# Optimization experiments

Measured on AMD Instinct MI355X. Metric: run time of the kernel, lower is better.

Reference implementation:

```python
import jax, jax.numpy as jnp
import numpy as np
from jax import lax

TAU = 10.0
THR = 1.0
ALPHA = float(np.exp(-1.0 / TAU))  # leak factor exp(-dt/tau), dt=1


def conv2d(x, w, pad):
    # x: [N,C,H,W], w: [O,I,kh,kw]
    return lax.conv_general_dilated(
        x, w, window_strides=(1, 1), padding=[(pad, pad), (pad, pad)],
        dimension_numbers=('NCHW', 'OIHW', 'NCHW'))


def avgpool(x, k):
    n, c, h, w = x.shape
    return x.reshape(n, c, h // k, k, w // k, k).mean(axis=(3, 5))


def exp_leak(x):
    # x: [T, ...]; v[t] = alpha*v[t-1] + x[t]; outputs membrane each step
    def step(v, xt):
        v = ALPHA * v + xt
        return v, v
    _, y = lax.scan(step, jnp.zeros_like(x[0]), x)
    return y


def lif(x):
    # LIF with SingleSpike + MembraneSubtract reset (norm_input=False)
    def step(v, xt):
        v = ALPHA * v + xt
        s = (v >= THR).astype(v.dtype)
        return v - s * THR, s
    _, s = lax.scan(step, jnp.zeros_like(x[0]), x)
    return s


def forward(x, conv1_w, conv2_w, lin_w):
    B, T = x.shape[:2]
    h = avgpool(conv2d(x.reshape(B * T, 2, 32, 32), conv1_w, 2), 4)  # [BT,4,8,8]
    h = h.reshape(B, T, 4, 8, 8).swapaxes(0, 1)                       # [T,B,4,8,8]
    h = lif(exp_leak(h)).swapaxes(0, 1).reshape(B * T, 4, 8, 8)
    h = avgpool(conv2d(h, conv2_w, 1), 2)                             # [BT,8,4,4]
    h = h.reshape(B, T, 8, 4, 4).swapaxes(0, 1)                       # [T,B,8,4,4]
    h = lif(exp_leak(h)).swapaxes(0, 1).reshape(B, T, 8 * 4 * 4)      # [B,T,128]
    return jnp.einsum('btf,of->bto', h, lin_w)                        # [B,T,2]


def setup_inputs() -> dict:
    key = jax.random.key(0)
    k1, k2, k3, k4 = jax.random.split(key, 4)
    B, T = 128, 100
    x = jax.random.uniform(k1, (B, T, 2, 32, 32), dtype=jnp.float32)
    conv1_w = jax.random.normal(k2, (4, 2, 5, 5), dtype=jnp.float32) / np.sqrt(2 * 5 * 5)
    conv2_w = jax.random.normal(k3, (8, 4, 3, 3), dtype=jnp.float32) / np.sqrt(4 * 3 * 3)
    lin_w = jax.random.normal(k4, (2, 128), dtype=jnp.float32) / np.sqrt(128)
    return {'x': x, 'conv1_w': conv1_w, 'conv2_w': conv2_w, 'lin_w': lin_w}


def reference(x, conv1_w, conv2_w, lin_w):
    return forward(x, conv1_w, conv2_w, lin_w)
```

## Files before the change

### kernel.cpp

```cpp
#include <hip/hip_runtime.h>

#define ALPHA 0.90483741803595957f

__global__ void prep_weights(const float* __restrict__ w1, const float* __restrict__ w2,
                             float* __restrict__ w1e, float* __restrict__ w2e) {
    int idx = blockIdx.x * 256 + threadIdx.x;
    if (idx < 512) {
        int v = idx & 7, u = (idx >> 3) & 7, ch = (idx >> 6) & 1, oc = idx >> 7;
        float s = 0.f;
        for (int a = 0; a < 5; ++a) {
            int i = u - a; if (i < 0 || i > 3) continue;
            for (int b = 0; b < 5; ++b) {
                int j = v - b; if (j < 0 || j > 3) continue;
                s += w1[((oc * 2 + ch) * 5 + a) * 5 + b];
            }
        }
        w1e[idx] = s * (1.f / 16.f);
    } else if (idx < 1024) {
        int k = idx - 512;
        int v = k & 3, u = (k >> 2) & 3, ch = (k >> 4) & 3, oc = k >> 6;
        float s = 0.f;
        for (int a = 0; a < 3; ++a) {
            int i = u - a; if (i < 0 || i > 1) continue;
            for (int b = 0; b < 3; ++b) {
                int j = v - b; if (j < 0 || j > 1) continue;
                s += w2[((oc * 4 + ch) * 3 + a) * 3 + b];
            }
        }
        w2e[k] = s * 0.25f;
    }
}

__global__ __launch_bounds__(256) void conv1_pool(const float* __restrict__ x,
                                                  const float* __restrict__ w1e,
                                                  float* __restrict__ y1) {
    __shared__ __align__(16) float tile[4][2][36][36];
    int tid = threadIdx.x;

    float4* t4 = (float4*)&tile[0][0][0][0];
    #pragma unroll
    for (int k = 0; k < 11; ++k) {
        int i = tid + k * 256;
        if (i < 2592) t4[i] = make_float4(0.f, 0.f, 0.f, 0.f);
    }
    __syncthreads();

    int li = tid >> 6, pos = tid & 63;
    long gi = (long)blockIdx.x * 4 + li;
    const float* src = x + gi * 2048;
    #pragma unroll
    for (int k = 0; k < 8; ++k) {
        int e = k * 256 + pos * 4;
        float4 d = *(const float4*)(src + e);
        int ch = e >> 10, rem = e & 1023, r = rem >> 5, c = rem & 31;
        float* dst = &tile[li][ch][r + 2][c + 2];
        dst[0] = d.x; dst[1] = d.y; dst[2] = d.z; dst[3] = d.w;
    }
    __syncthreads();

    int p = pos >> 3, q = pos & 7;
    float acc0 = 0.f, acc1 = 0.f, acc2 = 0.f, acc3 = 0.f;
    #pragma unroll
    for (int ch = 0; ch < 2; ++ch) {
        #pragma unroll
        for (int r = 0; r < 8; ++r) {
            const float* row = &tile[li][ch][4 * p + r][4 * q];
            float4 a = *(const float4*)row;
            float4 b = *(const float4*)(row + 4);
            float in[8] = {a.x, a.y, a.z, a.w, b.x, b.y, b.z, b.w};
            #pragma unroll
            for (int c = 0; c < 8; ++c) {
                float xi = in[c];
                acc0 += w1e[((0 * 2 + ch) * 8 + r) * 8 + c] * xi;
                acc1 += w1e[((1 * 2 + ch) * 8 + r) * 8 + c] * xi;
                acc2 += w1e[((2 * 2 + ch) * 8 + r) * 8 + c] * xi;
                acc3 += w1e[((3 * 2 + ch) * 8 + r) * 8 + c] * xi;
            }
        }
    }
    float* dst = y1 + gi * 256 + pos;
    dst[0] = acc0; dst[64] = acc1; dst[128] = acc2; dst[192] = acc3;
}

__global__ void scan1(const float* __restrict__ y1, float* __restrict__ spk) {
    int idx = blockIdx.x * 256 + threadIdx.x;
    int b = idx >> 8, f = idx & 255;
    const float* p = y1 + (long)b * 100 * 256 + f;
    float* o = spk + (long)b * 100 * 256 + f;
    float v1 = 0.f, v2 = 0.f;
    float xt = p[0];
    #pragma unroll 5
    for (int t = 0; t < 100; ++t) {
        float xn = (t < 99) ? p[(t + 1) * 256] : 0.f;
        v1 = ALPHA * v1 + xt;
        v2 = ALPHA * v2 + v1;
        float s = (v2 >= 1.f) ? 1.f : 0.f;
        o[t * 256] = s;
        v2 -= s;
        xt = xn;
    }
}

__global__ __launch_bounds__(256) void conv2_pool(const float* __restrict__ spk,
                                                  const float* __restrict__ w2e,
                                                  float* __restrict__ y2) {
    __shared__ __align__(16) float tile[2][4][10][10];
    int tid = threadIdx.x;
    float4* t4 = (float4*)&tile[0][0][0][0];
    if (tid < 200) t4[tid] = make_float4(0.f, 0.f, 0.f, 0.f);
    __syncthreads();

    const float* src = spk + (long)blockIdx.x * 512;
    #pragma unroll
    for (int k = 0; k < 2; ++k) {
        int e = k * 256 + tid;
        float d = src[e];
        int li = e >> 8, f = e & 255, ch = f >> 6, rem = f & 63, r = rem >> 3, c = rem & 7;
        tile[li][ch][r + 1][c + 1] = d;
    }
    __syncthreads();

    int li = tid >> 7, tpos = tid & 127;
    int oc = tpos >> 4, p = (tpos >> 2) & 3, q = tpos & 3;
    float acc = 0.f;
    #pragma unroll
    for (int ch = 0; ch < 4; ++ch) {
        #pragma unroll
        for (int r = 0; r < 4; ++r) {
            const float* row = &tile[li][ch][2 * p + r][2 * q];
            #pragma unroll
            for (int c = 0; c < 4; ++c)
                acc += w2e[((oc * 4 + ch) * 4 + r) * 4 + c] * row[c];
        }
    }
    long gi = (long)blockIdx.x * 2 + li;
    y2[gi * 128 + tpos] = acc;
}

__global__ void scan2(const float* __restrict__ y2, float* __restrict__ s2) {
    int idx = blockIdx.x * 256 + threadIdx.x;
    int b = idx >> 7, f = idx & 127;
    const float* p = y2 + (long)b * 100 * 128 + f;
    float* o = s2 + (long)b * 100 * 128 + f;
    float v1 = 0.f, v2 = 0.f;
    float xt = p[0];
    #pragma unroll 5
    for (int t = 0; t < 100; ++t) {
        float xn = (t < 99) ? p[(t + 1) * 128] : 0.f;
        v1 = ALPHA * v1 + xt;
        v2 = ALPHA * v2 + v1;
        float s = (v2 >= 1.f) ? 1.f : 0.f;
        o[t * 128] = s;
        v2 -= s;
        xt = xn;
    }
}

__global__ __launch_bounds__(256) void linear_out(const float* __restrict__ s2,
                                                  const float* __restrict__ lw,
                                                  float* __restrict__ out) {
    int tid = threadIdx.x;
    long bt = (long)blockIdx.x * 4 + (tid >> 6);
    int lane = tid & 63;
    float2 v = *(const float2*)(s2 + bt * 128 + lane * 2);
    float w00 = lw[lane * 2], w01 = lw[lane * 2 + 1];
    float w10 = lw[128 + lane * 2], w11 = lw[128 + lane * 2 + 1];
    float a0 = v.x * w00 + v.y * w01;
    float a1 = v.x * w10 + v.y * w11;
    #pragma unroll
    for (int off = 32; off; off >>= 1) {
        a0 += __shfl_down(a0, off);
        a1 += __shfl_down(a1, off);
    }
    if (lane == 0) { out[bt * 2] = a0; out[bt * 2 + 1] = a1; }
}

extern "C" void kernel_launch(void* const* d_in, const int* in_sizes, int n_in,
                              void* d_out, int out_size, void* d_ws, size_t ws_size,
                              hipStream_t stream) {
    const float* x  = (const float*)d_in[0];
    const float* w1 = (const float*)d_in[1];
    const float* w2 = (const float*)d_in[2];
    const float* lw = (const float*)d_in[3];
    float* out = (float*)d_out;

    float* ws   = (float*)d_ws;
    float* w1e  = ws;
    float* w2e  = ws + 512;
    float* bufA = ws + 1024;
    float* bufB = bufA + 3276800;

    prep_weights<<<4, 256, 0, stream>>>(w1, w2, w1e, w2e);
    conv1_pool<<<3200, 256, 0, stream>>>(x, w1e, bufA);
    scan1<<<128, 256, 0, stream>>>(bufA, bufB);
    conv2_pool<<<6400, 256, 0, stream>>>(bufB, w2e, bufA);
    scan2<<<64, 256, 0, stream>>>(bufA, bufB);
    linear_out<<<3200, 256, 0, stream>>>(bufB, lw, out);
}
```

Before: 209.7 us.

## Fuse scan1, conv2+pool, scan2 and linear into one per-batch kernel

Replaces the four post-conv1 kernels with one kernel, one block per batch element, that steps through time. Each step runs the first LIF scan, writes spikes to shared memory, computes conv2+pool from weights held in registers, runs the second scan, and applies the linear layer one step later on a double-buffered spike array. This removes the global round-trips of the intermediate spike and conv2 tensors and three launches. In exchange it serialises 100 timesteps with two block barriers each and runs only 128 blocks, so per-step latency and low occupancy may dominate.

```diff
diff --git a/kernel.cpp b/kernel.cpp
--- a/kernel.cpp
+++ b/kernel.cpp
@@ -82,97 +82,91 @@
     dst[0] = acc0; dst[64] = acc1; dst[128] = acc2; dst[192] = acc3;
 }
 
-__global__ void scan1(const float* __restrict__ y1, float* __restrict__ spk) {
-    int idx = blockIdx.x * 256 + threadIdx.x;
-    int b = idx >> 8, f = idx & 255;
-    const float* p = y1 + (long)b * 100 * 256 + f;
-    float* o = spk + (long)b * 100 * 256 + f;
-    float v1 = 0.f, v2 = 0.f;
-    float xt = p[0];
-    #pragma unroll 5
-    for (int t = 0; t < 100; ++t) {
-        float xn = (t < 99) ? p[(t + 1) * 256] : 0.f;
-        v1 = ALPHA * v1 + xt;
-        v2 = ALPHA * v2 + v1;
-        float s = (v2 >= 1.f) ? 1.f : 0.f;
-        o[t * 256] = s;
-        v2 -= s;
-        xt = xn;
+__global__ __launch_bounds__(256) void fused_rest(const float* __restrict__ y1,
+                                                  const float* __restrict__ w2e,
+                                                  const float* __restrict__ lw,
+                                                  float* __restrict__ out) {
+    __shared__ __align__(16) float spk[4][10][10];
+    __shared__ __align__(16) float s2buf[2][128];
+    __shared__ __align__(16) float outbuf[100][2];
+    int tid = threadIdx.x;
+    int b = blockIdx.x;
+
+    for (int i = tid; i < 400; i += 256) ((float*)spk)[i] = 0.f;
+
+    float wreg[64];
+    int g = tid, oc = g >> 4, p = (g >> 2) & 3, q = g & 3;
+    if (tid < 128) {
+        const float4* wsrc = (const float4*)(w2e + oc * 64);
+        #pragma unroll
+        for (int k = 0; k < 16; ++k) {
+            float4 w = wsrc[k];
+            wreg[4 * k] = w.x; wreg[4 * k + 1] = w.y;
+            wreg[4 * k + 2] = w.z; wreg[4 * k + 3] = w.w;
+        }
     }
-}
+    int lane = tid & 63;
+    float lwa = 0.f, lwb = 0.f;
+    if (tid >= 128) {
+        int o = (tid >> 6) - 2;
+        float2 lv = *(const float2*)(lw + o * 128 + 2 * lane);
+        lwa = lv.x; lwb = lv.y;
+    }
 
-__global__ __launch_bounds__(256) void conv2_pool(const float* __restrict__ spk,
-                                                  const float* __restrict__ w2e,
-                                                  float* __restrict__ y2) {
-    __shared__ __align__(16) float tile[2][4][10][10];
-    int tid = threadIdx.x;
-    float4* t4 = (float4*)&tile[0][0][0][0];
-    if (tid < 200) t4[tid] = make_float4(0.f, 0.f, 0.f, 0.f);
+    const float* yp = y1 + (long)b * 25600 + tid;
+    float v1a = 0.f, v1b = 0.f, v2a = 0.f, v2b = 0.f;
+    int ch = tid >> 6, r = (tid >> 3) & 7, c = tid & 7;
+
+    float xt = yp[0];
     __syncthreads();
 
-    const float* src = spk + (long)blockIdx.x * 512;
-    #pragma unroll
-    for (int k = 0; k < 2; ++k) {
-        int e = k * 256 + tid;
-        float d = src[e];
-        int li = e >> 8, f = e & 255, ch = f >> 6, rem = f & 63, r = rem >> 3, c = rem & 7;
-        tile[li][ch][r + 1][c + 1] = d;
+    for (int t = 0; t < 100; ++t) {
+        float xn = (t < 99) ? yp[(t + 1) * 256] : 0.f;
+        v1a = ALPHA * v1a + xt;
+        v1b = ALPHA * v1b + v1a;
+        float s = (v1b >= 1.f) ? 1.f : 0.f;
+        v1b -= s;
+        spk[ch][r + 1][c + 1] = s;
+        xt = xn;
+        __syncthreads();
+        if (tid < 128) {
+            float acc = 0.f;
+            #pragma unroll
+            for (int cc = 0; cc < 4; ++cc) {
+                #pragma unroll
+                for (int rr = 0; rr < 4; ++rr) {
+                    const float* rowp = &spk[cc][2 * p + rr][2 * q];
+                    float2 a = *(const float2*)rowp;
+                    float2 bb = *(const float2*)(rowp + 2);
+                    int wb = cc * 16 + rr * 4;
+                    acc += wreg[wb] * a.x + wreg[wb + 1] * a.y
+                         + wreg[wb + 2] * bb.x + wreg[wb + 3] * bb.y;
+                }
+            }
+            v2a = ALPHA * v2a + acc;
+            v2b = ALPHA * v2b + v2a;
+            float s2 = (v2b >= 1.f) ? 1.f : 0.f;
+            v2b -= s2;
+            s2buf[t & 1][g] = s2;
+        } else if (t > 0) {
+            float2 sv = *(const float2*)&s2buf[(t - 1) & 1][2 * lane];
+            float pa = sv.x * lwa + sv.y * lwb;
+            #pragma unroll
+            for (int off = 32; off; off >>= 1) pa += __shfl_down(pa, off);
+            if (lane == 0) outbuf[t - 1][(tid >> 6) - 2] = pa;
+        }
+        __syncthreads();
+    }
+    if (tid >= 128) {
+        float2 sv = *(const float2*)&s2buf[1][2 * lane];
+        float pa = sv.x * lwa + sv.y * lwb;
+        #pragma unroll
+        for (int off = 32; off; off >>= 1) pa += __shfl_down(pa, off);
+        if (lane == 0) outbuf[99][(tid >> 6) - 2] = pa;
     }
     __syncthreads();
-
-    int li = tid >> 7, tpos = tid & 127;
-    int oc = tpos >> 4, p = (tpos >> 2) & 3, q = tpos & 3;
-    float acc = 0.f;
-    #pragma unroll
-    for (int ch = 0; ch < 4; ++ch) {
-        #pragma unroll
-        for (int r = 0; r < 4; ++r) {
-            const float* row = &tile[li][ch][2 * p + r][2 * q];
-            #pragma unroll
-            for (int c = 0; c < 4; ++c)
-                acc += w2e[((oc * 4 + ch) * 4 + r) * 4 + c] * row[c];
-        }
-    }
-    long gi = (long)blockIdx.x * 2 + li;
-    y2[gi * 128 + tpos] = acc;
-}
-
-__global__ void scan2(const float* __restrict__ y2, float* __restrict__ s2) {
-    int idx = blockIdx.x * 256 + threadIdx.x;
-    int b = idx >> 7, f = idx & 127;
-    const float* p = y2 + (long)b * 100 * 128 + f;
-    float* o = s2 + (long)b * 100 * 128 + f;
-    float v1 = 0.f, v2 = 0.f;
-    float xt = p[0];
-    #pragma unroll 5
-    for (int t = 0; t < 100; ++t) {
-        float xn = (t < 99) ? p[(t + 1) * 128] : 0.f;
-        v1 = ALPHA * v1 + xt;
-        v2 = ALPHA * v2 + v1;
-        float s = (v2 >= 1.f) ? 1.f : 0.f;
-        o[t * 128] = s;
-        v2 -= s;
-        xt = xn;
-    }
-}
-
-__global__ __launch_bounds__(256) void linear_out(const float* __restrict__ s2,
-                                                  const float* __restrict__ lw,
-                                                  float* __restrict__ out) {
-    int tid = threadIdx.x;
-    long bt = (long)blockIdx.x * 4 + (tid >> 6);
-    int lane = tid & 63;
-    float2 v = *(const float2*)(s2 + bt * 128 + lane * 2);
-    float w00 = lw[lane * 2], w01 = lw[lane * 2 + 1];
-    float w10 = lw[128 + lane * 2], w11 = lw[128 + lane * 2 + 1];
-    float a0 = v.x * w00 + v.y * w01;
-    float a1 = v.x * w10 + v.y * w11;
-    #pragma unroll
-    for (int off = 32; off; off >>= 1) {
-        a0 += __shfl_down(a0, off);
-        a1 += __shfl_down(a1, off);
-    }
-    if (lane == 0) { out[bt * 2] = a0; out[bt * 2 + 1] = a1; }
+    float* op = out + (long)b * 200;
+    if (tid < 200) op[tid] = ((float*)outbuf)[tid];
 }
 
 extern "C" void kernel_launch(void* const* d_in, const int* in_sizes, int n_in,
@@ -184,16 +178,12 @@
     const float* lw = (const float*)d_in[3];
     float* out = (float*)d_out;
 
-    float* ws   = (float*)d_ws;
-    float* w1e  = ws;
-    float* w2e  = ws + 512;
-    float* bufA = ws + 1024;
-    float* bufB = bufA + 3276800;
+    float* ws  = (float*)d_ws;
+    float* w1e = ws;
+    float* w2e = ws + 512;
+    float* y1  = ws + 1024;
 
     prep_weights<<<4, 256, 0, stream>>>(w1, w2, w1e, w2e);
-    conv1_pool<<<3200, 256, 0, stream>>>(x, w1e, bufA);
-    scan1<<<128, 256, 0, stream>>>(bufA, bufB);
-    conv2_pool<<<6400, 256, 0, stream>>>(bufB, w2e, bufA);
-    scan2<<<64, 256, 0, stream>>>(bufA, bufB);
-    linear_out<<<3200, 256, 0, stream>>>(bufB, lw, out);
+    conv1_pool<<<3200, 256, 0, stream>>>(x, w1e, y1);
+    fused_rest<<<128, 256, 0, stream>>>(y1, w2e, lw, out);
 }
```

Result: slower. 231.3 us (+10.3%).
